# Performance work log

Measured on AMD Instinct MI355X. Metric: run time of the kernel, lower is better.

## Reference

```python
import jax, jax.numpy as jnp
import numpy as np

B, T_ENC, D_IN, H, C, STEPS = 512, 64, 512, 512, 38, 26


def setup_inputs() -> dict:
    key = jax.random.key(0)
    ks = jax.random.split(key, 12)
    s = 0.05
    return {
        "encoder_output": jax.random.normal(ks[0], (B, T_ENC, D_IN), jnp.float32),
        "text": jax.random.randint(ks[1], (B, STEPS), 0, C),
        "w_i2h": jax.random.normal(ks[2], (H, D_IN), jnp.float32) * s,
        "w_h2h": jax.random.normal(ks[3], (H, H), jnp.float32) * s,
        "b_h2h": jax.random.normal(ks[4], (H,), jnp.float32) * s,
        "w_score": jax.random.normal(ks[5], (1, H), jnp.float32) * s,
        "w_ih": jax.random.normal(ks[6], (4 * H, D_IN + C), jnp.float32) * s,
        "w_hh": jax.random.normal(ks[7], (4 * H, H), jnp.float32) * s,
        "b_ih": jax.random.normal(ks[8], (4 * H,), jnp.float32) * s,
        "b_hh": jax.random.normal(ks[9], (4 * H,), jnp.float32) * s,
        "w_gen": jax.random.normal(ks[10], (C, H), jnp.float32) * s,
        "b_gen": jax.random.normal(ks[11], (C,), jnp.float32) * s,
    }


def reference(encoder_output, text, w_i2h, w_h2h, b_h2h, w_score, w_ih, w_hh,
              b_ih, b_hh, w_gen, b_gen):
    # i2h(batch_H) is step-invariant -> hoist out of the decode loop (same math).
    H_proj = jnp.einsum('btd,hd->bth', encoder_output, w_i2h)  # [B,T,H]
    onehots = jax.nn.one_hot(text, C, dtype=encoder_output.dtype)  # [B,S,C]
    oh_seq = jnp.swapaxes(onehots, 0, 1)  # [S,B,C]

    def step(carry, oh):
        h, c = carry
        hp = (h @ w_h2h.T + b_h2h)[:, None, :]                 # [B,1,H]
        e = jnp.tanh(H_proj + hp) @ w_score[0]                  # [B,T]
        alpha = jax.nn.softmax(e, axis=1)                       # [B,T]
        context = jnp.einsum('bt,btd->bd', alpha, encoder_output)
        x = jnp.concatenate([context, oh], axis=1)              # [B,D+C]
        gates = x @ w_ih.T + b_ih + h @ w_hh.T + b_hh           # [B,4H]
        i_g, f_g, g_g, o_g = jnp.split(gates, 4, axis=1)
        c_new = jax.nn.sigmoid(f_g) * c + jax.nn.sigmoid(i_g) * jnp.tanh(g_g)
        h_new = jax.nn.sigmoid(o_g) * jnp.tanh(c_new)
        return (h_new, c_new), h_new

    z = jnp.zeros((encoder_output.shape[0], w_h2h.shape[0]), encoder_output.dtype)
    _, hs = jax.lax.scan(step, (z, z), oh_seq)                  # hs: [S,B,H]
    hiddens = jnp.swapaxes(hs, 0, 1)                            # [B,S,H]
    probs = hiddens @ w_gen.T + b_gen                           # [B,S,C]
    return probs
```

## Files before the change

kernel.cpp:

```cpp
#include <hip/hip_runtime.h>

typedef __attribute__((ext_vector_type(8))) short bf16x8;
typedef __attribute__((ext_vector_type(4))) float f32x4;
typedef __attribute__((ext_vector_type(4))) int   i32x4;

#define DEV static __device__ __forceinline__

constexpr int BATCH = 512;
constexpr int TENC  = 64;
constexpr int DIN   = 512;
constexpr int HDIM  = 512;
constexpr int NCLS  = 38;
constexpr int STEPS = 26;
constexpr int NG    = 4 * HDIM;

constexpr size_t HP_OFF   = 0;
constexpr size_t HP_SZ    = (size_t)BATCH * TENC * HDIM * 2;
constexpr size_t ENC_OFF  = HP_OFF + HP_SZ;
constexpr size_t ENC_SZ   = (size_t)BATCH * TENC * DIN * 2;
constexpr size_t A2_OFF   = ENC_OFF + ENC_SZ;
constexpr size_t A2_SZ    = (size_t)2 * BATCH * 1024 * 2;
constexpr size_t HP32_OFF = A2_OFF + A2_SZ;
constexpr size_t HP32_SZ  = (size_t)BATCH * HDIM * 4;
constexpr size_t B2R_OFF  = HP32_OFF + HP32_SZ;
constexpr size_t B2R_SZ   = (size_t)NG * 1024 * 2;
constexpr size_t WI2H_OFF = B2R_OFF + B2R_SZ;
constexpr size_t WI2H_SZ  = (size_t)HDIM * DIN * 2;
constexpr size_t B3_OFF   = WI2H_OFF + WI2H_SZ;
constexpr size_t B3_SZ    = (size_t)576 * HDIM * 2;
constexpr size_t WOH_OFF  = B3_OFF + B3_SZ;
constexpr size_t WOH_SZ   = (size_t)NG * NCLS * 4;
constexpr size_t BIAS_OFF = WOH_OFF + WOH_SZ;
constexpr size_t BIAS_SZ  = (size_t)NG * 4;
constexpr size_t HSEQ_OFF = BIAS_OFF + BIAS_SZ;
constexpr size_t HSEQ_SZ  = (size_t)STEPS * BATCH * HDIM * 2;
constexpr size_t BAR_OFF  = HSEQ_OFF + HSEQ_SZ;
constexpr size_t BAR_SZ   = 32768;

DEV float bf2f(unsigned short s) {
    unsigned u = ((unsigned)s) << 16;
    return __builtin_bit_cast(float, u);
}
DEV unsigned short f2bf(float f) {
    unsigned u = __builtin_bit_cast(unsigned, f);
    u = (u + 0x7fffu + ((u >> 16) & 1u)) >> 16;
    return (unsigned short)u;
}
DEV float sigmoid_f(float x) { return 1.f / (1.f + __expf(-x)); }
DEV float tanh_f(float x) {
    x = fminf(fmaxf(x, -15.f), 15.f);
    float e = __expf(2.f * x);
    return (e - 1.f) / (e + 1.f);
}

DEV unsigned aload(const unsigned* p) {
    return __hip_atomic_load(p, __ATOMIC_RELAXED, __HIP_MEMORY_SCOPE_AGENT);
}
DEV unsigned long long aload64(const unsigned long long* p) {
    return __hip_atomic_load(p, __ATOMIC_RELAXED, __HIP_MEMORY_SCOPE_AGENT);
}
DEV float aloadf(const float* p) {
    return __hip_atomic_load(p, __ATOMIC_RELAXED, __HIP_MEMORY_SCOPE_AGENT);
}
DEV void astore(unsigned* p, unsigned v) {
    __hip_atomic_store(p, v, __ATOMIC_RELAXED, __HIP_MEMORY_SCOPE_AGENT);
}
DEV void astoref(float* p, float v) {
    __hip_atomic_store(p, v, __ATOMIC_RELAXED, __HIP_MEMORY_SCOPE_AGENT);
}
DEV bf16x8 mk_frag(unsigned long long lo, unsigned long long hi) {
    union { unsigned long long q[2]; bf16x8 v; } u;
    u.q[0] = lo; u.q[1] = hi;
    return u.v;
}

DEV void gbar_arrive(unsigned* ctr) {
    __syncthreads();
    if (threadIdx.x == 0)
        __hip_atomic_fetch_add(ctr, 1u, __ATOMIC_RELAXED, __HIP_MEMORY_SCOPE_AGENT);
}
DEV void gbar_wait(unsigned* ctr, unsigned g) {
    if (threadIdx.x == 0) {
        while (aload(ctr) < g * 32u) __builtin_amdgcn_s_sleep(1);
    }
    __syncthreads();
}

__global__ void conv_bf16_kernel(const float* __restrict__ in,
                                 unsigned short* __restrict__ out, int n4) {
    int i = blockIdx.x * blockDim.x + threadIdx.x;
    int stride = gridDim.x * blockDim.x;
    for (; i < n4; i += stride) {
        float4 v = ((const float4*)in)[i];
        ushort4 o;
        o.x = f2bf(v.x); o.y = f2bf(v.y); o.z = f2bf(v.z); o.w = f2bf(v.w);
        ((ushort4*)out)[i] = o;
    }
}

__global__ void build_b2r_kernel(const float* __restrict__ w_ih, const float* __restrict__ w_hh,
                                 const float* __restrict__ b_ih, const float* __restrict__ b_hh,
                                 unsigned short* __restrict__ B2r, float* __restrict__ woh,
                                 float* __restrict__ bias2r) {
    int np = blockIdx.x;
    int u = np >> 2, g = np & 3;
    int src = g * 512 + u;
    for (int k = threadIdx.x; k < 512; k += blockDim.x) {
        B2r[np * 1024 + k]       = f2bf(w_ih[src * 550 + k]);
        B2r[np * 1024 + 512 + k] = f2bf(w_hh[src * 512 + k]);
    }
    if (threadIdx.x < NCLS) woh[np * NCLS + threadIdx.x] = w_ih[src * 550 + 512 + threadIdx.x];
    if (threadIdx.x == 0)   bias2r[np] = b_ih[src] + b_hh[src];
}

__global__ void build_b3_kernel(const float* __restrict__ w_h2h, const float* __restrict__ w_gen,
                                unsigned short* __restrict__ B3) {
    int n = blockIdx.x;
    for (int k = threadIdx.x; k < 512; k += blockDim.x) {
        float v = 0.f;
        if (n < 512)      v = w_h2h[n * 512 + k];
        else if (n < 550) v = w_gen[(n - 512) * 512 + k];
        B3[n * 512 + k] = f2bf(v);
    }
}

__global__ void init_state_kernel(unsigned short* __restrict__ A2,
                                  unsigned* __restrict__ bar) {
    int b = blockIdx.x;
    for (int j = threadIdx.x; j < 512; j += blockDim.x)
        A2[b * 1024 + 512 + j] = 0;
    if (b == 0)
        for (int j = threadIdx.x; j < 8192; j += blockDim.x) bar[j] = 0;
}

template<int BM, int BN, int WN, int FRM, int FRN>
DEV void gemm_core(const unsigned short* __restrict__ A, int ldA,
                   const unsigned short* __restrict__ Bm, int ldB, int K,
                   int m0, int n0, unsigned short* __restrict__ lA,
                   unsigned short* __restrict__ lB, f32x4 acc[FRM][FRN]) {
    constexpr int LSTR = 40;
    const int tid  = threadIdx.x;
    const int lane = tid & 63;
    const int wid  = tid >> 6;
    const int wm = wid / WN, wn = wid % WN;
    const int fr_row = lane & 15;
    const int fr_kb  = (lane >> 4) * 8;

    for (int k0 = 0; k0 < K; k0 += 32) {
        for (int u = tid; u < BM * 4; u += 256) {
            int r = u >> 2, cb = u & 3;
            *(i32x4*)(lA + r * LSTR + cb * 8) =
                *(const i32x4*)(A + (size_t)(m0 + r) * ldA + k0 + cb * 8);
        }
        for (int u = tid; u < BN * 4; u += 256) {
            int r = u >> 2, cb = u & 3;
            *(i32x4*)(lB + r * LSTR + cb * 8) =
                *(const i32x4*)(Bm + (size_t)(n0 + r) * ldB + k0 + cb * 8);
        }
        __syncthreads();
        bf16x8 af[FRM], bfv[FRN];
        #pragma unroll
        for (int i = 0; i < FRM; i++)
            af[i] = *(const bf16x8*)(lA + (wm * FRM * 16 + i * 16 + fr_row) * LSTR + fr_kb);
        #pragma unroll
        for (int j = 0; j < FRN; j++)
            bfv[j] = *(const bf16x8*)(lB + (wn * FRN * 16 + j * 16 + fr_row) * LSTR + fr_kb);
        #pragma unroll
        for (int i = 0; i < FRM; i++)
            #pragma unroll
            for (int j = 0; j < FRN; j++)
                acc[i][j] = __builtin_amdgcn_mfma_f32_16x16x32_bf16(af[i], bfv[j], acc[i][j], 0, 0, 0);
        __syncthreads();
    }
}

__global__ __launch_bounds__(256) void gemm_bf16out_kernel(
    const unsigned short* __restrict__ A, int ldA,
    const unsigned short* __restrict__ Bm, int ldB,
    unsigned short* __restrict__ C, int ldC, int K) {
    constexpr int BM = 128, BN = 128, FRM = 4, FRN = 4;
    __shared__ __align__(16) unsigned short lA[BM * 40], lB[BN * 40];
    int m0 = blockIdx.x * BM, n0 = blockIdx.y * BN;
    f32x4 acc[FRM][FRN] = {};
    gemm_core<BM, BN, 2, FRM, FRN>(A, ldA, Bm, ldB, K, m0, n0, lA, lB, acc);
    const int lane = threadIdx.x & 63, wid = threadIdx.x >> 6;
    const int wm = wid >> 1, wn = wid & 1;
    #pragma unroll
    for (int i = 0; i < FRM; i++)
        #pragma unroll
        for (int j = 0; j < FRN; j++)
            #pragma unroll
            for (int r = 0; r < 4; r++) {
                int m = m0 + wm * FRM * 16 + i * 16 + (lane >> 4) * 4 + r;
                int n = n0 + wn * FRN * 16 + j * 16 + (lane & 15);
                C[(size_t)m * ldC + n] = f2bf(acc[i][j][r]);
            }
}

__global__ __launch_bounds__(256) void probs_kernel(
    const unsigned short* __restrict__ hseq,
    const unsigned short* __restrict__ Bg,
    const float* __restrict__ b_gen, float* __restrict__ out) {
    __shared__ __align__(16) unsigned short lA[64 * 40], lB[64 * 40];
    int m0 = blockIdx.x * 64;
    f32x4 acc[2][2] = {};
    gemm_core<64, 64, 2, 2, 2>(hseq, 512, Bg, 512, 512, m0, 0, lA, lB, acc);
    const int lane = threadIdx.x & 63, wid = threadIdx.x >> 6;
    const int wm = wid >> 1, wn = wid & 1;
    #pragma unroll
    for (int i = 0; i < 2; i++)
        #pragma unroll
        for (int j = 0; j < 2; j++)
            #pragma unroll
            for (int r = 0; r < 4; r++) {
                int m = m0 + wm * 32 + i * 16 + (lane >> 4) * 4 + r;
                int n = wn * 32 + j * 16 + (lane & 15);
                if (n < NCLS) {
                    int ss = m >> 9, b = m & 511;
                    out[((size_t)b * STEPS + ss) * NCLS + n] = acc[i][j][r] + b_gen[n];
                }
            }
}

__global__ __launch_bounds__(512) void decode_kernel(
    const unsigned short* __restrict__ Hp,
    const unsigned short* __restrict__ enc,
    unsigned short* __restrict__ A2,
    float* __restrict__ hpb,
    const unsigned short* __restrict__ B2r,
    const float* __restrict__ bias2r,
    const float* __restrict__ woh,
    const unsigned short* __restrict__ B3,
    const float* __restrict__ b_h2h,
    const float* __restrict__ w_score,
    const int* __restrict__ text,
    unsigned short* __restrict__ hseq,
    unsigned* __restrict__ bar) {
    __shared__ __align__(16) unsigned short lB2w[64 * 1032];
    __shared__ __align__(16) char scr[17408];

    const int bid  = blockIdx.x;
    const int tid  = threadIdx.x;
    const int lane = tid & 63, wid = tid >> 6;
    const int grp = bid >> 5;
    const int j   = bid & 31;
    const int gm0 = grp * 64;
    const int ng0 = j * 64;
    const int ncol0 = j * 16;
    const int mi = wid & 3;
    const int kh = wid >> 2;
    unsigned* ctr = bar + grp * 256;

    for (int u = tid; u < 8192; u += 512) {
        int r = u >> 7, cb = u & 127;
        *(i32x4*)(lB2w + r * 1032 + cb * 8) =
            *(const i32x4*)(B2r + (size_t)(ng0 + r) * 1024 + cb * 8);
    }

    float c0 = 0.f, c1 = 0.f;
    unsigned gen = 0;

    float* pbuf  = (float*)scr;
    float* e_lds = (float*)scr;
    float* al_lds = e_lds + 128;
    float* gbuf  = (float*)scr;

    const int half = tid >> 8, t4 = tid & 255, w4 = t4 >> 6;
    const int ab = gm0 + 2 * j + half;

    for (int s = 0; s < STEPS; ++s) {
        unsigned short* A2cur = A2 + (size_t)(s & 1) * BATCH * 1024;
        unsigned short* A2nxt = A2 + (size_t)((s + 1) & 1) * BATCH * 1024;

        unsigned long long h0v[8], h1v[8];
        {
            const unsigned long long* Ah = (const unsigned long long*)
                (A2cur + (size_t)(gm0 + mi * 16 + (lane & 15)) * 1024 + 512
                 + kh * 256 + (lane >> 4) * 8);
            #pragma unroll
            for (int kc = 0; kc < 8; ++kc) {
                h0v[kc] = aload64(Ah + kc * 8);
                h1v[kc] = aload64(Ah + kc * 8 + 1);
            }
            const unsigned short* wrow = B3 + (size_t)(ncol0 + (lane & 15)) * 512
                                            + kh * 256 + (lane >> 4) * 8;
            f32x4 acc = {};
            #pragma unroll
            for (int kc = 0; kc < 8; ++kc) {
                bf16x8 af = mk_frag(h0v[kc], h1v[kc]);
                bf16x8 bf = *(const bf16x8*)(wrow + kc * 32);
                acc = __builtin_amdgcn_mfma_f32_16x16x32_bf16(af, bf, acc, 0, 0, 0);
            }
            if (kh == 1) {
                #pragma unroll
                for (int r = 0; r < 4; r++)
                    pbuf[mi * 272 + ((lane >> 4) * 4 + r) * 17 + (lane & 15)] = acc[r];
            }
            __syncthreads();
            if (kh == 0) {
                #pragma unroll
                for (int r = 0; r < 4; r++) {
                    int row = (lane >> 4) * 4 + r, col = lane & 15;
                    float v = acc[r] + pbuf[mi * 272 + row * 17 + col] + b_h2h[ncol0 + col];
                    astoref(hpb + (size_t)(gm0 + mi * 16 + row) * 512 + ncol0 + col, v);
                }
            }
        }
        gbar_arrive(ctr); ++gen;

        bf16x8 hpv[16];
        #pragma unroll
        for (int tt = 0; tt < 16; ++tt) {
            int t = w4 + tt * 4;
            hpv[tt] = *(const bf16x8*)(Hp + ((size_t)ab * 64 + t) * 512 + lane * 8);
        }
        f32x4 gacc[4] = {};
        #pragma unroll
        for (int kc = 0; kc < 8; ++kc) {
            bf16x8 af = mk_frag(h0v[kc], h1v[kc]);
            #pragma unroll
            for (int nj = 0; nj < 4; ++nj) {
                bf16x8 bf = *(const bf16x8*)(lB2w + (nj * 16 + (lane & 15)) * 1032
                                             + 512 + kh * 256 + (lane >> 4) * 8 + kc * 32);
                gacc[nj] = __builtin_amdgcn_mfma_f32_16x16x32_bf16(af, bf, gacc[nj], 0, 0, 0);
            }
        }
        gbar_wait(ctr, gen);

        {
            float hp8[8], ws8[8];
            #pragma unroll
            for (int q = 0; q < 8; q++) hp8[q] = aloadf(hpb + (size_t)ab * 512 + lane * 8 + q);
            {
                const float4* wsp = (const float4*)(w_score + lane * 8);
                float4 w0 = wsp[0], w1 = wsp[1];
                ws8[0] = w0.x; ws8[1] = w0.y; ws8[2] = w0.z; ws8[3] = w0.w;
                ws8[4] = w1.x; ws8[5] = w1.y; ws8[6] = w1.z; ws8[7] = w1.w;
            }
            #pragma unroll
            for (int tt = 0; tt < 16; ++tt) {
                int t = w4 + tt * 4;
                float a = 0.f;
                #pragma unroll
                for (int q = 0; q < 8; q++)
                    a += ws8[q] * tanh_f(hp8[q] + bf2f((unsigned short)hpv[tt][q]));
                #pragma unroll
                for (int off = 32; off > 0; off >>= 1) a += __shfl_down(a, off);
                if (lane == 0) e_lds[half * 64 + t] = a;
            }
            __syncthreads();
            if (w4 == 0) {
                float v = e_lds[half * 64 + lane];
                float m = v;
                #pragma unroll
                for (int off = 32; off > 0; off >>= 1) m = fmaxf(m, __shfl_xor(m, off));
                float ex = __expf(v - m);
                float sum = ex;
                #pragma unroll
                for (int off = 32; off > 0; off >>= 1) sum += __shfl_xor(sum, off);
                al_lds[half * 64 + lane] = ex / sum;
            }
            __syncthreads();
            float a0 = 0.f, a1 = 0.f;
            const unsigned short* erow = enc + (size_t)ab * 64 * 512 + t4 * 2;
            #pragma unroll 8
            for (int t = 0; t < 64; t++) {
                float al = al_lds[half * 64 + t];
                unsigned pv = *(const unsigned*)(erow + (size_t)t * 512);
                a0 += al * bf2f((unsigned short)(pv & 0xffffu));
                a1 += al * bf2f((unsigned short)(pv >> 16));
            }
            unsigned pk = ((unsigned)f2bf(a1) << 16) | (unsigned)f2bf(a0);
            astore((unsigned*)(A2cur + (size_t)ab * 1024) + t4, pk);
        }
        gbar_arrive(ctr); ++gen;
        gbar_wait(ctr, gen);

        {
            const unsigned long long* Ac = (const unsigned long long*)
                (A2cur + (size_t)(gm0 + mi * 16 + (lane & 15)) * 1024
                 + kh * 256 + (lane >> 4) * 8);
            unsigned long long c0v[8], c1v[8];
            #pragma unroll
            for (int kc = 0; kc < 8; ++kc) {
                c0v[kc] = aload64(Ac + kc * 8);
                c1v[kc] = aload64(Ac + kc * 8 + 1);
            }
            #pragma unroll
            for (int kc = 0; kc < 8; ++kc) {
                bf16x8 af = mk_frag(c0v[kc], c1v[kc]);
                #pragma unroll
                for (int nj = 0; nj < 4; ++nj) {
                    bf16x8 bf = *(const bf16x8*)(lB2w + (nj * 16 + (lane & 15)) * 1032
                                                 + kh * 256 + (lane >> 4) * 8 + kc * 32);
                    gacc[nj] = __builtin_amdgcn_mfma_f32_16x16x32_bf16(af, bf, gacc[nj], 0, 0, 0);
                }
            }
            const int grow = mi * 16 + (lane >> 4) * 4;
            const int gcol = lane & 15;
            if (kh == 1) {
                #pragma unroll
                for (int nj = 0; nj < 4; ++nj)
                    #pragma unroll
                    for (int r = 0; r < 4; r++)
                        gbuf[(grow + r) * 68 + nj * 16 + gcol] = gacc[nj][r];
            }
            __syncthreads();
            if (kh == 0) {
                #pragma unroll
                for (int nj = 0; nj < 4; ++nj)
                    #pragma unroll
                    for (int r = 0; r < 4; r++)
                        gbuf[(grow + r) * 68 + nj * 16 + gcol] += gacc[nj][r];
            }
            __syncthreads();
            {
                const int rl = tid >> 3, q = tid & 7;
                const int b = gm0 + rl;
                const int npb = ng0 + q * 8;
                const int u0 = npb >> 2;
                const int tb = text[b * STEPS + s];
                const float* gr = gbuf + rl * 68 + q * 8;
                float4 g0 = *(const float4*)gr;
                float4 g1 = *(const float4*)(gr + 4);
                float vi0 = g0.x + bias2r[npb + 0] + woh[(npb + 0) * NCLS + tb];
                float vf0 = g0.y + bias2r[npb + 1] + woh[(npb + 1) * NCLS + tb];
                float vg0 = g0.z + bias2r[npb + 2] + woh[(npb + 2) * NCLS + tb];
                float vo0 = g0.w + bias2r[npb + 3] + woh[(npb + 3) * NCLS + tb];
                float vi1 = g1.x + bias2r[npb + 4] + woh[(npb + 4) * NCLS + tb];
                float vf1 = g1.y + bias2r[npb + 5] + woh[(npb + 5) * NCLS + tb];
                float vg1 = g1.z + bias2r[npb + 6] + woh[(npb + 6) * NCLS + tb];
                float vo1 = g1.w + bias2r[npb + 7] + woh[(npb + 7) * NCLS + tb];
                float cn0 = sigmoid_f(vf0) * c0 + sigmoid_f(vi0) * tanh_f(vg0);
                float cn1 = sigmoid_f(vf1) * c1 + sigmoid_f(vi1) * tanh_f(vg1);
                c0 = cn0; c1 = cn1;
                float hn0 = sigmoid_f(vo0) * tanh_f(cn0);
                float hn1 = sigmoid_f(vo1) * tanh_f(cn1);
                unsigned hp2 = ((unsigned)f2bf(hn1) << 16) | (unsigned)f2bf(hn0);
                astore((unsigned*)(A2nxt + (size_t)b * 1024 + 512 + u0), hp2);
                *(unsigned*)(hseq + ((size_t)s * BATCH + b) * 512 + u0) = hp2;
            }
        }
        if (s + 1 < STEPS) {
            gbar_arrive(ctr); ++gen;
            gbar_wait(ctr, gen);
        }
    }
}

extern "C" void kernel_launch(void* const* d_in, const int* in_sizes, int n_in,
                              void* d_out, int out_size, void* d_ws, size_t ws_size,
                              hipStream_t stream) {
    (void)in_sizes; (void)n_in; (void)out_size; (void)ws_size;
    const float* enc_f   = (const float*)d_in[0];
    const int*   text    = (const int*)d_in[1];
    const float* w_i2h   = (const float*)d_in[2];
    const float* w_h2h   = (const float*)d_in[3];
    const float* b_h2h   = (const float*)d_in[4];
    const float* w_score = (const float*)d_in[5];
    const float* w_ih    = (const float*)d_in[6];
    const float* w_hh    = (const float*)d_in[7];
    const float* b_ih    = (const float*)d_in[8];
    const float* b_hh    = (const float*)d_in[9];
    const float* w_gen   = (const float*)d_in[10];
    const float* b_gen   = (const float*)d_in[11];
    float* out = (float*)d_out;

    char* ws = (char*)d_ws;
    const unsigned short* Hp     = (const unsigned short*)(ws + HP_OFF);
    unsigned short*       Hp_w   = (unsigned short*)(ws + HP_OFF);
    const unsigned short* encb   = (const unsigned short*)(ws + ENC_OFF);
    unsigned short*       encb_w = (unsigned short*)(ws + ENC_OFF);
    unsigned short*       A2     = (unsigned short*)(ws + A2_OFF);
    float*                hpb    = (float*)(ws + HP32_OFF);
    const unsigned short* B2r    = (const unsigned short*)(ws + B2R_OFF);
    unsigned short*       B2r_w  = (unsigned short*)(ws + B2R_OFF);
    unsigned short*       wi2hb  = (unsigned short*)(ws + WI2H_OFF);
    const unsigned short* B3     = (const unsigned short*)(ws + B3_OFF);
    unsigned short*       B3_w   = (unsigned short*)(ws + B3_OFF);
    const float*          woh    = (const float*)(ws + WOH_OFF);
    float*                woh_w  = (float*)(ws + WOH_OFF);
    const float*          bias2r = (const float*)(ws + BIAS_OFF);
    float*                bias2r_w = (float*)(ws + BIAS_OFF);
    unsigned short*       hseq   = (unsigned short*)(ws + HSEQ_OFF);
    unsigned*             bar    = (unsigned*)(ws + BAR_OFF);

    conv_bf16_kernel<<<2048, 256, 0, stream>>>(enc_f, encb_w, BATCH * TENC * DIN / 4);
    conv_bf16_kernel<<<256, 256, 0, stream>>>(w_i2h, wi2hb, HDIM * DIN / 4);
    build_b2r_kernel<<<NG, 256, 0, stream>>>(w_ih, w_hh, b_ih, b_hh, B2r_w, woh_w, bias2r_w);
    build_b3_kernel<<<576, 256, 0, stream>>>(w_h2h, w_gen, B3_w);
    init_state_kernel<<<BATCH, 256, 0, stream>>>(A2, bar);

    gemm_bf16out_kernel<<<dim3(BATCH * TENC / 128, HDIM / 128), 256, 0, stream>>>(
        encb, DIN, wi2hb, DIN, Hp_w, HDIM, DIN);

    {
        void* args[13] = {
            (void*)&Hp, (void*)&encb, (void*)&A2, (void*)&hpb,
            (void*)&B2r, (void*)&bias2r, (void*)&woh, (void*)&B3,
            (void*)&b_h2h, (void*)&w_score, (void*)&text, (void*)&hseq, (void*)&bar
        };
        hipLaunchCooperativeKernel((const void*)decode_kernel, dim3(256), dim3(512),
                                   args, 0, stream);
    }

    probs_kernel<<<dim3(STEPS * BATCH / 64), 256, 0, stream>>>(
        hseq, B3 + (size_t)512 * 512, b_gen, out);
}
```

Measured before the change: 1.228 ms.

## Split each block group into two half-batches with staggered barriers to overlap phases

```diff
diff --git a/kernel.cpp b/kernel.cpp
--- a/kernel.cpp
+++ b/kernel.cpp
@@ -237,45 +237,50 @@
     unsigned short* __restrict__ hseq,
     unsigned* __restrict__ bar) {
     __shared__ __align__(16) unsigned short lB2w[64 * 1032];
-    __shared__ __align__(16) char scr[17408];
+    __shared__ __align__(16) float pbuf[2 * 16 * 17];
+    __shared__ __align__(16) float e_lds[64];
+    __shared__ __align__(16) float al_lds[64];
+    __shared__ __align__(16) float gbuf[32 * 68];
 
     const int bid  = blockIdx.x;
     const int tid  = threadIdx.x;
     const int lane = tid & 63, wid = tid >> 6;
-    const int grp = bid >> 5;
+    const int q   = bid >> 5;
     const int j   = bid & 31;
-    const int gm0 = grp * 64;
+    const int gm0A = q * 64;
+    const int gm0B = q * 64 + 32;
     const int ng0 = j * 64;
     const int ncol0 = j * 16;
-    const int mi = wid & 3;
-    const int kh = wid >> 2;
-    unsigned* ctr = bar + grp * 256;
+    const int gsel = wid >> 2;
+    const int wloc = wid & 3;
+    const int mi = wloc & 1;
+    const int kh = wloc >> 1;
+    const int gm0w = gsel ? gm0B : gm0A;
+    unsigned* ctrA = bar + (q * 2) * 32;
+    unsigned* ctrB = bar + (q * 2 + 1) * 32;
+    const int abA = gm0A + j, abB = gm0B + j;
 
     for (int u = tid; u < 8192; u += 512) {
         int r = u >> 7, cb = u & 127;
         *(i32x4*)(lB2w + r * 1032 + cb * 8) =
             *(const i32x4*)(B2r + (size_t)(ng0 + r) * 1024 + cb * 8);
     }
+    __syncthreads();
 
     float c0 = 0.f, c1 = 0.f;
-    unsigned gen = 0;
-
-    float* pbuf  = (float*)scr;
-    float* e_lds = (float*)scr;
-    float* al_lds = e_lds + 128;
-    float* gbuf  = (float*)scr;
-
-    const int half = tid >> 8, t4 = tid & 255, w4 = t4 >> 6;
-    const int ab = gm0 + 2 * j + half;
+    unsigned genA = 0, genB = 0;
 
     for (int s = 0; s < STEPS; ++s) {
         unsigned short* A2cur = A2 + (size_t)(s & 1) * BATCH * 1024;
         unsigned short* A2nxt = A2 + (size_t)((s + 1) & 1) * BATCH * 1024;
 
         unsigned long long h0v[8], h1v[8];
-        {
+        f32x4 gacc[4] = {};
+
+        gbar_wait(ctrA, genA);
+        if (gsel == 0) {
             const unsigned long long* Ah = (const unsigned long long*)
-                (A2cur + (size_t)(gm0 + mi * 16 + (lane & 15)) * 1024 + 512
+                (A2cur + (size_t)(gm0A + mi * 16 + (lane & 15)) * 1024 + 512
                  + kh * 256 + (lane >> 4) * 8);
             #pragma unroll
             for (int kc = 0; kc < 8; ++kc) {
@@ -302,19 +307,52 @@
                 for (int r = 0; r < 4; r++) {
                     int row = (lane >> 4) * 4 + r, col = lane & 15;
                     float v = acc[r] + pbuf[mi * 272 + row * 17 + col] + b_h2h[ncol0 + col];
-                    astoref(hpb + (size_t)(gm0 + mi * 16 + row) * 512 + ncol0 + col, v);
-                }
-            }
-        }
-        gbar_arrive(ctr); ++gen;
-
-        bf16x8 hpv[16];
-        #pragma unroll
-        for (int tt = 0; tt < 16; ++tt) {
-            int t = w4 + tt * 4;
-            hpv[tt] = *(const bf16x8*)(Hp + ((size_t)ab * 64 + t) * 512 + lane * 8);
-        }
-        f32x4 gacc[4] = {};
+                    astoref(hpb + (size_t)(gm0A + mi * 16 + row) * 512 + ncol0 + col, v);
+                }
+            }
+        } else {
+            __syncthreads();
+        }
+        gbar_arrive(ctrA); ++genA;
+
+        gbar_wait(ctrB, genB);
+        if (gsel == 1) {
+            const unsigned long long* Ah = (const unsigned long long*)
+                (A2cur + (size_t)(gm0B + mi * 16 + (lane & 15)) * 1024 + 512
+                 + kh * 256 + (lane >> 4) * 8);
+            #pragma unroll
+            for (int kc = 0; kc < 8; ++kc) {
+                h0v[kc] = aload64(Ah + kc * 8);
+                h1v[kc] = aload64(Ah + kc * 8 + 1);
+            }
+            const unsigned short* wrow = B3 + (size_t)(ncol0 + (lane & 15)) * 512
+                                            + kh * 256 + (lane >> 4) * 8;
+            f32x4 acc = {};
+            #pragma unroll
+            for (int kc = 0; kc < 8; ++kc) {
+                bf16x8 af = mk_frag(h0v[kc], h1v[kc]);
+                bf16x8 bf = *(const bf16x8*)(wrow + kc * 32);
+                acc = __builtin_amdgcn_mfma_f32_16x16x32_bf16(af, bf, acc, 0, 0, 0);
+            }
+            if (kh == 1) {
+                #pragma unroll
+                for (int r = 0; r < 4; r++)
+                    pbuf[mi * 272 + ((lane >> 4) * 4 + r) * 17 + (lane & 15)] = acc[r];
+            }
+            __syncthreads();
+            if (kh == 0) {
+                #pragma unroll
+                for (int r = 0; r < 4; r++) {
+                    int row = (lane >> 4) * 4 + r, col = lane & 15;
+                    float v = acc[r] + pbuf[mi * 272 + row * 17 + col] + b_h2h[ncol0 + col];
+                    astoref(hpb + (size_t)(gm0B + mi * 16 + row) * 512 + ncol0 + col, v);
+                }
+            }
+        } else {
+            __syncthreads();
+        }
+        gbar_arrive(ctrB); ++genB;
+
         #pragma unroll
         for (int kc = 0; kc < 8; ++kc) {
             bf16x8 af = mk_frag(h0v[kc], h1v[kc]);
@@ -325,32 +363,33 @@
                 gacc[nj] = __builtin_amdgcn_mfma_f32_16x16x32_bf16(af, bf, gacc[nj], 0, 0, 0);
             }
         }
-        gbar_wait(ctr, gen);
-
+
+        bf16x8 hpv[8];
+        #pragma unroll
+        for (int tt = 0; tt < 8; ++tt)
+            hpv[tt] = *(const bf16x8*)(Hp + ((size_t)abA * 64 + wid * 8 + tt) * 512 + lane * 8);
+        gbar_wait(ctrA, genA);
         {
             float hp8[8], ws8[8];
             #pragma unroll
-            for (int q = 0; q < 8; q++) hp8[q] = aloadf(hpb + (size_t)ab * 512 + lane * 8 + q);
-            {
-                const float4* wsp = (const float4*)(w_score + lane * 8);
-                float4 w0 = wsp[0], w1 = wsp[1];
-                ws8[0] = w0.x; ws8[1] = w0.y; ws8[2] = w0.z; ws8[3] = w0.w;
-                ws8[4] = w1.x; ws8[5] = w1.y; ws8[6] = w1.z; ws8[7] = w1.w;
-            }
-            #pragma unroll
-            for (int tt = 0; tt < 16; ++tt) {
-                int t = w4 + tt * 4;
+            for (int q8 = 0; q8 < 8; q8++) hp8[q8] = aloadf(hpb + (size_t)abA * 512 + lane * 8 + q8);
+            const float4* wsp = (const float4*)(w_score + lane * 8);
+            float4 w0 = wsp[0], w1 = wsp[1];
+            ws8[0] = w0.x; ws8[1] = w0.y; ws8[2] = w0.z; ws8[3] = w0.w;
+            ws8[4] = w1.x; ws8[5] = w1.y; ws8[6] = w1.z; ws8[7] = w1.w;
+            #pragma unroll
+            for (int tt = 0; tt < 8; ++tt) {
                 float a = 0.f;
                 #pragma unroll
-                for (int q = 0; q < 8; q++)
-                    a += ws8[q] * tanh_f(hp8[q] + bf2f((unsigned short)hpv[tt][q]));
+                for (int q8 = 0; q8 < 8; q8++)
+                    a += ws8[q8] * tanh_f(hp8[q8] + bf2f((unsigned short)hpv[tt][q8]));
                 #pragma unroll
                 for (int off = 32; off > 0; off >>= 1) a += __shfl_down(a, off);
-                if (lane == 0) e_lds[half * 64 + t] = a;
-            }
-            __syncthreads();
-            if (w4 == 0) {
-                float v = e_lds[half * 64 + lane];
+                if (lane == 0) e_lds[wid * 8 + tt] = a;
+            }
+            __syncthreads();
+            if (wid == 0) {
+                float v = e_lds[lane];
                 float m = v;
                 #pragma unroll
                 for (int off = 32; off > 0; off >>= 1) m = fmaxf(m, __shfl_xor(m, off));
@@ -358,55 +397,110 @@
                 float sum = ex;
                 #pragma unroll
                 for (int off = 32; off > 0; off >>= 1) sum += __shfl_xor(sum, off);
-                al_lds[half * 64 + lane] = ex / sum;
-            }
-            __syncthreads();
-            float a0 = 0.f, a1 = 0.f;
-            const unsigned short* erow = enc + (size_t)ab * 64 * 512 + t4 * 2;
-            #pragma unroll 8
-            for (int t = 0; t < 64; t++) {
-                float al = al_lds[half * 64 + t];
-                unsigned pv = *(const unsigned*)(erow + (size_t)t * 512);
-                a0 += al * bf2f((unsigned short)(pv & 0xffffu));
-                a1 += al * bf2f((unsigned short)(pv >> 16));
-            }
-            unsigned pk = ((unsigned)f2bf(a1) << 16) | (unsigned)f2bf(a0);
-            astore((unsigned*)(A2cur + (size_t)ab * 1024) + t4, pk);
-        }
-        gbar_arrive(ctr); ++gen;
-        gbar_wait(ctr, gen);
-
+                al_lds[lane] = ex / sum;
+            }
+            __syncthreads();
+            if (tid < 256) {
+                float a0 = 0.f, a1 = 0.f;
+                const unsigned short* erow = enc + (size_t)abA * 64 * 512 + tid * 2;
+                #pragma unroll 8
+                for (int t = 0; t < 64; t++) {
+                    float al = al_lds[t];
+                    unsigned pv = *(const unsigned*)(erow + (size_t)t * 512);
+                    a0 += al * bf2f((unsigned short)(pv & 0xffffu));
+                    a1 += al * bf2f((unsigned short)(pv >> 16));
+                }
+                unsigned pk = ((unsigned)f2bf(a1) << 16) | (unsigned)f2bf(a0);
+                astore((unsigned*)(A2cur + (size_t)abA * 1024) + tid, pk);
+            }
+        }
+        gbar_arrive(ctrA); ++genA;
+
+        #pragma unroll
+        for (int tt = 0; tt < 8; ++tt)
+            hpv[tt] = *(const bf16x8*)(Hp + ((size_t)abB * 64 + wid * 8 + tt) * 512 + lane * 8);
+        gbar_wait(ctrB, genB);
         {
-            const unsigned long long* Ac = (const unsigned long long*)
-                (A2cur + (size_t)(gm0 + mi * 16 + (lane & 15)) * 1024
-                 + kh * 256 + (lane >> 4) * 8);
-            unsigned long long c0v[8], c1v[8];
-            #pragma unroll
-            for (int kc = 0; kc < 8; ++kc) {
-                c0v[kc] = aload64(Ac + kc * 8);
-                c1v[kc] = aload64(Ac + kc * 8 + 1);
-            }
-            #pragma unroll
-            for (int kc = 0; kc < 8; ++kc) {
-                bf16x8 af = mk_frag(c0v[kc], c1v[kc]);
-                #pragma unroll
-                for (int nj = 0; nj < 4; ++nj) {
-                    bf16x8 bf = *(const bf16x8*)(lB2w + (nj * 16 + (lane & 15)) * 1032
-                                                 + kh * 256 + (lane >> 4) * 8 + kc * 32);
-                    gacc[nj] = __builtin_amdgcn_mfma_f32_16x16x32_bf16(af, bf, gacc[nj], 0, 0, 0);
-                }
-            }
-            const int grow = mi * 16 + (lane >> 4) * 4;
-            const int gcol = lane & 15;
-            if (kh == 1) {
-                #pragma unroll
-                for (int nj = 0; nj < 4; ++nj)
+            float hp8[8], ws8[8];
+            #pragma unroll
+            for (int q8 = 0; q8 < 8; q8++) hp8[q8] = aloadf(hpb + (size_t)abB * 512 + lane * 8 + q8);
+            const float4* wsp = (const float4*)(w_score + lane * 8);
+            float4 w0 = wsp[0], w1 = wsp[1];
+            ws8[0] = w0.x; ws8[1] = w0.y; ws8[2] = w0.z; ws8[3] = w0.w;
+            ws8[4] = w1.x; ws8[5] = w1.y; ws8[6] = w1.z; ws8[7] = w1.w;
+            #pragma unroll
+            for (int tt = 0; tt < 8; ++tt) {
+                float a = 0.f;
+                #pragma unroll
+                for (int q8 = 0; q8 < 8; q8++)
+                    a += ws8[q8] * tanh_f(hp8[q8] + bf2f((unsigned short)hpv[tt][q8]));
+                #pragma unroll
+                for (int off = 32; off > 0; off >>= 1) a += __shfl_down(a, off);
+                if (lane == 0) e_lds[wid * 8 + tt] = a;
+            }
+            __syncthreads();
+            if (wid == 0) {
+                float v = e_lds[lane];
+                float m = v;
+                #pragma unroll
+                for (int off = 32; off > 0; off >>= 1) m = fmaxf(m, __shfl_xor(m, off));
+                float ex = __expf(v - m);
+                float sum = ex;
+                #pragma unroll
+                for (int off = 32; off > 0; off >>= 1) sum += __shfl_xor(sum, off);
+                al_lds[lane] = ex / sum;
+            }
+            __syncthreads();
+            if (tid < 256) {
+                float a0 = 0.f, a1 = 0.f;
+                const unsigned short* erow = enc + (size_t)abB * 64 * 512 + tid * 2;
+                #pragma unroll 8
+                for (int t = 0; t < 64; t++) {
+                    float al = al_lds[t];
+                    unsigned pv = *(const unsigned*)(erow + (size_t)t * 512);
+                    a0 += al * bf2f((unsigned short)(pv & 0xffffu));
+                    a1 += al * bf2f((unsigned short)(pv >> 16));
+                }
+                unsigned pk = ((unsigned)f2bf(a1) << 16) | (unsigned)f2bf(a0);
+                astore((unsigned*)(A2cur + (size_t)abB * 1024) + tid, pk);
+            }
+        }
+        gbar_arrive(ctrB); ++genB;
+
+        gbar_wait(ctrA, genA);
+        {
+            if (gsel == 0) {
+                const unsigned long long* Ac = (const unsigned long long*)
+                    (A2cur + (size_t)(gm0A + mi * 16 + (lane & 15)) * 1024
+                     + kh * 256 + (lane >> 4) * 8);
+                unsigned long long c0v[8], c1v[8];
+                #pragma unroll
+                for (int kc = 0; kc < 8; ++kc) {
+                    c0v[kc] = aload64(Ac + kc * 8);
+                    c1v[kc] = aload64(Ac + kc * 8 + 1);
+                }
+                #pragma unroll
+                for (int kc = 0; kc < 8; ++kc) {
+                    bf16x8 af = mk_frag(c0v[kc], c1v[kc]);
                     #pragma unroll
-                    for (int r = 0; r < 4; r++)
-                        gbuf[(grow + r) * 68 + nj * 16 + gcol] = gacc[nj][r];
-            }
-            __syncthreads();
-            if (kh == 0) {
+                    for (int nj = 0; nj < 4; ++nj) {
+                        bf16x8 bf = *(const bf16x8*)(lB2w + (nj * 16 + (lane & 15)) * 1032
+                                                     + kh * 256 + (lane >> 4) * 8 + kc * 32);
+                        gacc[nj] = __builtin_amdgcn_mfma_f32_16x16x32_bf16(af, bf, gacc[nj], 0, 0, 0);
+                    }
+                }
+                if (kh == 1) {
+                    const int grow = mi * 16 + (lane >> 4) * 4, gcol = lane & 15;
+                    #pragma unroll
+                    for (int nj = 0; nj < 4; ++nj)
+                        #pragma unroll
+                        for (int r = 0; r < 4; r++)
+                            gbuf[(grow + r) * 68 + nj * 16 + gcol] = gacc[nj][r];
+                }
+            }
+            __syncthreads();
+            if (gsel == 0 && kh == 0) {
+                const int grow = mi * 16 + (lane >> 4) * 4, gcol = lane & 15;
                 #pragma unroll
                 for (int nj = 0; nj < 4; ++nj)
                     #pragma unroll
@@ -414,13 +508,13 @@
                         gbuf[(grow + r) * 68 + nj * 16 + gcol] += gacc[nj][r];
             }
             __syncthreads();
-            {
-                const int rl = tid >> 3, q = tid & 7;
-                const int b = gm0 + rl;
-                const int npb = ng0 + q * 8;
+            if (tid < 256) {
+                const int rl = tid >> 3, q8 = tid & 7;
+                const int b = gm0A + rl;
+                const int npb = ng0 + q8 * 8;
                 const int u0 = npb >> 2;
                 const int tb = text[b * STEPS + s];
-                const float* gr = gbuf + rl * 68 + q * 8;
+                const float* gr = gbuf + rl * 68 + q8 * 8;
                 float4 g0 = *(const float4*)gr;
                 float4 g1 = *(const float4*)(gr + 4);
                 float vi0 = g0.x + bias2r[npb + 0] + woh[(npb + 0) * NCLS + tb];
@@ -441,10 +535,78 @@
                 *(unsigned*)(hseq + ((size_t)s * BATCH + b) * 512 + u0) = hp2;
             }
         }
-        if (s + 1 < STEPS) {
-            gbar_arrive(ctr); ++gen;
-            gbar_wait(ctr, gen);
-        }
+        gbar_arrive(ctrA); ++genA;
+
+        gbar_wait(ctrB, genB);
+        {
+            if (gsel == 1) {
+                const unsigned long long* Ac = (const unsigned long long*)
+                    (A2cur + (size_t)(gm0B + mi * 16 + (lane & 15)) * 1024
+                     + kh * 256 + (lane >> 4) * 8);
+                unsigned long long c0v[8], c1v[8];
+                #pragma unroll
+                for (int kc = 0; kc < 8; ++kc) {
+                    c0v[kc] = aload64(Ac + kc * 8);
+                    c1v[kc] = aload64(Ac + kc * 8 + 1);
+                }
+                #pragma unroll
+                for (int kc = 0; kc < 8; ++kc) {
+                    bf16x8 af = mk_frag(c0v[kc], c1v[kc]);
+                    #pragma unroll
+                    for (int nj = 0; nj < 4; ++nj) {
+                        bf16x8 bf = *(const bf16x8*)(lB2w + (nj * 16 + (lane & 15)) * 1032
+                                                     + kh * 256 + (lane >> 4) * 8 + kc * 32);
+                        gacc[nj] = __builtin_amdgcn_mfma_f32_16x16x32_bf16(af, bf, gacc[nj], 0, 0, 0);
+                    }
+                }
+                if (kh == 1) {
+                    const int grow = mi * 16 + (lane >> 4) * 4, gcol = lane & 15;
+                    #pragma unroll
+                    for (int nj = 0; nj < 4; ++nj)
+                        #pragma unroll
+                        for (int r = 0; r < 4; r++)
+                            gbuf[(grow + r) * 68 + nj * 16 + gcol] = gacc[nj][r];
+                }
+            }
+            __syncthreads();
+            if (gsel == 1 && kh == 0) {
+                const int grow = mi * 16 + (lane >> 4) * 4, gcol = lane & 15;
+                #pragma unroll
+                for (int nj = 0; nj < 4; ++nj)
+                    #pragma unroll
+                    for (int r = 0; r < 4; r++)
+                        gbuf[(grow + r) * 68 + nj * 16 + gcol] += gacc[nj][r];
+            }
+            __syncthreads();
+            if (tid >= 256) {
+                const int t2 = tid - 256;
+                const int rl = t2 >> 3, q8 = t2 & 7;
+                const int b = gm0B + rl;
+                const int npb = ng0 + q8 * 8;
+                const int u0 = npb >> 2;
+                const int tb = text[b * STEPS + s];
+                const float* gr = gbuf + rl * 68 + q8 * 8;
+                float4 g0 = *(const float4*)gr;
+                float4 g1 = *(const float4*)(gr + 4);
+                float vi0 = g0.x + bias2r[npb + 0] + woh[(npb + 0) * NCLS + tb];
+                float vf0 = g0.y + bias2r[npb + 1] + woh[(npb + 1) * NCLS + tb];
+                float vg0 = g0.z + bias2r[npb + 2] + woh[(npb + 2) * NCLS + tb];
+                float vo0 = g0.w + bias2r[npb + 3] + woh[(npb + 3) * NCLS + tb];
+                float vi1 = g1.x + bias2r[npb + 4] + woh[(npb + 4) * NCLS + tb];
+                float vf1 = g1.y + bias2r[npb + 5] + woh[(npb + 5) * NCLS + tb];
+                float vg1 = g1.z + bias2r[npb + 6] + woh[(npb + 6) * NCLS + tb];
+                float vo1 = g1.w + bias2r[npb + 7] + woh[(npb + 7) * NCLS + tb];
+                float cn0 = sigmoid_f(vf0) * c0 + sigmoid_f(vi0) * tanh_f(vg0);
+                float cn1 = sigmoid_f(vf1) * c1 + sigmoid_f(vi1) * tanh_f(vg1);
+                c0 = cn0; c1 = cn1;
+                float hn0 = sigmoid_f(vo0) * tanh_f(cn0);
+                float hn1 = sigmoid_f(vo1) * tanh_f(cn1);
+                unsigned hp2 = ((unsigned)f2bf(hn1) << 16) | (unsigned)f2bf(hn0);
+                astore((unsigned*)(A2nxt + (size_t)b * 1024 + 512 + u0), hp2);
+                *(unsigned*)(hseq + ((size_t)s * BATCH + b) * 512 + u0) = hp2;
+            }
+        }
+        gbar_arrive(ctrB); ++genB;
     }
 }
 
```

Result: slower. 2.094 ms (+70.6%).
